# Performance work log

Measured on AMD Instinct MI355X. Metric: run time of the kernel, lower is better.

The kernel has to match this reference:

```python
import jax, jax.numpy as jnp
import numpy as np

B, N_IN, NV, F = 1, 65536, 1, 64
N_OUT, K = 16384, 16
N_DIST, N_PHI, OUT = 4, 8, 256
DIST_MAX = 0.1  # grid_layers[level_out].min_dist stand-in


def setup_inputs() -> dict:
    key = jax.random.key(0)
    ks = jax.random.split(key, 6)
    x = jax.random.normal(ks[0], (B, N_IN, NV, F), dtype=jnp.float32)
    nh_idx = jax.random.randint(ks[1], (N_OUT, K), 0, N_IN)  # neighbor gather indices
    d_dists = jax.random.uniform(ks[2], (N_OUT, K), dtype=jnp.float32) * DIST_MAX
    d_phi = jax.random.uniform(ks[3], (N_OUT, K), dtype=jnp.float32) * (2 * np.pi) - np.pi
    dists = jnp.linspace(0.0, DIST_MAX, N_DIST, dtype=jnp.float32)          # anchor distances
    sigma = jnp.asarray(DIST_MAX / 2, dtype=jnp.float32)                     # n_sigma == 1 -> scalar
    phi = jnp.linspace(-np.pi, np.pi, N_PHI + 1, dtype=jnp.float32)[:-1]     # von Mises: phi_min = -pi
    kappa = jnp.asarray(1.0, dtype=jnp.float32)                              # kappa_init
    W_out = jax.random.normal(ks[4], (F * N_DIST * N_PHI, OUT), dtype=jnp.float32) / np.sqrt(F * N_DIST * N_PHI)
    return {"x": x, "d_dists": d_dists, "d_phi": d_phi, "dists": dists,
            "sigma": sigma, "kappa": kappa, "phi": phi, "W_out": W_out, "nh_idx": nh_idx}


def reference(x, d_dists, d_phi, dists, sigma, kappa, phi, W_out, nh_idx):
    # Gaussian distance kernel: exp(-0.5*((d - dist_k)/sigma)^2)  -> (N_OUT, K, N_DIST)
    w_d = jnp.exp(-0.5 * ((d_dists[..., None] - dists) / sigma) ** 2)
    # von Mises angular kernel: exp(kappa * cos(d_phi - phi_p))   -> (N_OUT, K, N_PHI)
    w_p = jnp.exp(kappa * jnp.cos(d_phi[..., None] - phi))
    # combined kernel weights, normalized over the K neighbors per anchor
    w = w_d[..., :, None] * w_p[..., None, :]                      # (N_OUT, K, N_DIST, N_PHI)
    w = w / (jnp.sum(w, axis=1, keepdims=True) + 1e-9)
    w = w.reshape(N_OUT, K, N_DIST * N_PHI)                        # (N_OUT, K, M)
    # gather neighbor features from the input grid
    x_nb = x[:, nh_idx]                                            # (B, N_OUT, K, NV, F)
    # weighted aggregation over neighbors -> enhanced channels
    agg = jnp.einsum('bnkvf,nkm->bnvmf', x_nb, w)                  # (B, N_OUT, NV, M, F)
    agg = agg.reshape(B, N_OUT, NV, N_DIST * N_PHI * F)            # model_dim_enhanced = 2048
    return agg @ W_out                                             # (B, N_OUT, NV, OUT)
```

## Files before the change

### kernel.cpp

```cpp
#include <hip/hip_runtime.h>
#include <hip/hip_bf16.h>

#define N_IN   65536
#define N_OUTP 16384
#define KNB    16
#define FDIM   64
#define M_DIM  32
#define KDIM   2048
#define OUT_D  256

typedef __bf16 bf16x8_t __attribute__((ext_vector_type(8)));
typedef float  f32x4_t  __attribute__((ext_vector_type(4)));
typedef float  f32x2_t  __attribute__((ext_vector_type(2)));


__device__ __forceinline__ unsigned pk2(float a, float b) {
  __bf16 b0 = (__bf16)a, b1 = (__bf16)b;
  return ((unsigned)__builtin_bit_cast(unsigned short, b1) << 16) |
          (unsigned)__builtin_bit_cast(unsigned short, b0);
}

__global__ __launch_bounds__(256) void pack_B_kernel(
    const float* __restrict__ W, uint4* __restrict__ Bws)
{
  __shared__ float wlds[32 * 260];
  const int kk = blockIdx.x;
  const int t  = threadIdx.x;

  const float4* Wb = (const float4*)(W + kk * 32 * OUT_D);
#pragma unroll
  for (int i = 0; i < 8; ++i) {
    int idx = i * 256 + t;
    int row = idx >> 6, c4 = idx & 63;
    float4 v = Wb[idx];
    *(float4*)(wlds + row * 260 + c4 * 4) = v;
  }
  __syncthreads();

#pragma unroll
  for (int j = 0; j < 4; ++j) {
    int c  = j * 256 + t;
    int l  = c & 63, nt = c >> 6;
    int r0 = (l >> 4) * 8, col = nt * 16 + (l & 15);
    union { unsigned short s[8]; uint4 v; } u;
#pragma unroll
    for (int jj = 0; jj < 8; ++jj) {
      __bf16 b = (__bf16)wlds[(r0 + jj) * 260 + col];
      u.s[jj] = __builtin_bit_cast(unsigned short, b);
    }
    Bws[(size_t)kk * 1024 + c] = u.v;
  }
}

#define WST 580
#define WKS 36
#define XST 1092
#define XKS 68

__global__ __launch_bounds__(256) void agg_kernel(
    const float* __restrict__ x,
    const float* __restrict__ d_dists,
    const float* __restrict__ d_phi,
    const float* __restrict__ dists,
    const float* __restrict__ sigma_p,
    const float* __restrict__ kappa_p,
    const float* __restrict__ phi,
    const int*   __restrict__ nh_idx,
    uint4*       __restrict__ Aws)
{
  __shared__ __align__(16) float wbuf[8 * WST];
  __shared__ __align__(16) float xbuf[8 * XST];

  const int t  = threadIdx.x;
  const int n0 = blockIdx.x * 8;
  const int T  = blockIdx.x >> 1;
  const int r0 = (blockIdx.x & 1) * 8;

  const int h = t & 1, gk = (t >> 1) & 15, gr8 = t >> 5;
  const int gidx = nh_idx[(n0 + gr8) * KNB + gk];
  const float4* xr = (const float4*)x + (size_t)gidx * 16 + h * 8;
  float4 xreg[8];
#pragma unroll
  for (int j = 0; j < 8; ++j) xreg[j] = xr[j];

  {
    const float sinv = 1.0f / sigma_p[0];
    const float kap  = kappa_p[0];
    float phiv[8], distv[4];
#pragma unroll
    for (int p = 0; p < 8; ++p) phiv[p] = phi[p];
#pragma unroll
    for (int d = 0; d < 4; ++d) distv[d] = dists[d];

    int rk = t >> 1, r8 = rk >> 4, k = rk & 15, rep = t & 1;
    int n = n0 + r8;
    float dd = d_dists[n * KNB + k];
    float dp = d_phi[n * KNB + k];
    float wp[8];
#pragma unroll
    for (int p = 0; p < 8; ++p) wp[p] = __expf(kap * __cosf(dp - phiv[p]));
#pragma unroll
    for (int dl = 0; dl < 2; ++dl) {
      int d = rep * 2 + dl;
      float td = (dd - distv[d]) * sinv;
      float wd = __expf(-0.5f * td * td);
      float* dst = wbuf + r8 * WST + k * WKS + d * 8;
      *(float4*)(dst)     = make_float4(wd * wp[0], wd * wp[1], wd * wp[2], wd * wp[3]);
      *(float4*)(dst + 4) = make_float4(wd * wp[4], wd * wp[5], wd * wp[6], wd * wp[7]);
    }
  }

  {
    float4* xd = (float4*)(xbuf + gr8 * XST + gk * XKS + h * 36);
#pragma unroll
    for (int j = 0; j < 8; ++j) xd[j] = xreg[j];
  }
  __syncthreads();

  {
    int r8 = t >> 5, m = t & 31;
    float wv[16];
    float s = 0.f;
#pragma unroll
    for (int k = 0; k < 16; ++k) {
      wv[k] = wbuf[r8 * WST + k * WKS + m];
      s += wv[k];
    }
    float wn = 1.0f / (s + 1e-9f);
#pragma unroll
    for (int k = 0; k < 16; ++k)
      wbuf[r8 * WST + k * WKS + m] = wv[k] * wn;
  }
  __syncthreads();

  {
    const int r8 = t & 7, fo = (t >> 3) & 7, mq = t >> 6;
    f32x2_t acc[8][4];
#pragma unroll
    for (int mi = 0; mi < 8; ++mi)
#pragma unroll
      for (int fj = 0; fj < 4; ++fj) acc[mi][fj] = (f32x2_t){0.f, 0.f};

    const float* wp_ = wbuf + r8 * WST + mq * 8;
    const float* xp_ = xbuf + r8 * XST + ((fo < 4) ? fo * 8 : 36 + (fo - 4) * 8);

#pragma unroll 8
    for (int k = 0; k < 16; ++k) {
      float4 wa = *(const float4*)(wp_ + k * WKS);
      float4 wb = *(const float4*)(wp_ + k * WKS + 4);
      float4 xa = *(const float4*)(xp_ + k * XKS);
      float4 xb = *(const float4*)(xp_ + k * XKS + 4);
      float wv[8] = {wa.x, wa.y, wa.z, wa.w, wb.x, wb.y, wb.z, wb.w};
      f32x2_t xv[4] = {(f32x2_t){xa.x, xa.y}, (f32x2_t){xa.z, xa.w},
                       (f32x2_t){xb.x, xb.y}, (f32x2_t){xb.z, xb.w}};
#pragma unroll
      for (int mi = 0; mi < 8; ++mi) {
        f32x2_t wm = (f32x2_t){wv[mi], wv[mi]};
#pragma unroll
        for (int fj = 0; fj < 4; ++fj)
          acc[mi][fj] += wm * xv[fj];
      }
    }

    uint4* base = Aws + (size_t)T * 4096 + (fo & 3) * 16 + r0 + r8
                      + (size_t)(fo >> 2) * 64;
#pragma unroll
    for (int mi = 0; mi < 8; ++mi) {
      int m = mq * 8 + mi;
      uint4 v;
      v.x = pk2(acc[mi][0][0], acc[mi][0][1]);
      v.y = pk2(acc[mi][1][0], acc[mi][1][1]);
      v.z = pk2(acc[mi][2][0], acc[mi][2][1]);
      v.w = pk2(acc[mi][3][0], acc[mi][3][1]);
      base[m * 128] = v;
    }
  }
}

__global__ __launch_bounds__(512, 2) void gemm_kernel(
    const uint4* __restrict__ Astream,
    const uint4* __restrict__ Bws,
    float*       __restrict__ out)
{
  __shared__ float red[4][64 * 68];

  const int t    = threadIdx.x;
  const int lane = t & 63;
  const int w    = t >> 6;
  const int cg   = w & 3;
  const int half = w >> 2;
  const int rb   = blockIdx.x;

  const uint4* pa = Astream + (size_t)(rb * 4) * 4096 + half * 64 + lane;
  const uint4* pb = Bws + (half * 16 + cg * 4) * 64 + lane;

  f32x4_t cacc[4][4];
#pragma unroll
  for (int mt = 0; mt < 4; ++mt)
#pragma unroll
    for (int i = 0; i < 4; ++i)
      cacc[mt][i] = (f32x4_t){0.f, 0.f, 0.f, 0.f};

  uint4 a[4][4], b[4][4];
#pragma unroll
  for (int s = 0; s < 4; ++s) {
#pragma unroll
    for (int mt = 0; mt < 4; ++mt) a[s][mt] = pa[mt * 4096 + s * 128];
#pragma unroll
    for (int i = 0; i < 4; ++i)    b[s][i]  = pb[s * 2048 + i * 64];
  }

#pragma unroll 4
  for (int j = 0; j < 32; ++j) {
    const int s = j & 3;
    bf16x8_t B0 = __builtin_bit_cast(bf16x8_t, b[s][0]);
    bf16x8_t B1 = __builtin_bit_cast(bf16x8_t, b[s][1]);
    bf16x8_t B2 = __builtin_bit_cast(bf16x8_t, b[s][2]);
    bf16x8_t B3 = __builtin_bit_cast(bf16x8_t, b[s][3]);
#pragma unroll
    for (int mt = 0; mt < 4; ++mt) {
      bf16x8_t A = __builtin_bit_cast(bf16x8_t, a[s][mt]);
      cacc[mt][0] = __builtin_amdgcn_mfma_f32_16x16x32_bf16(A, B0, cacc[mt][0], 0, 0, 0);
      cacc[mt][1] = __builtin_amdgcn_mfma_f32_16x16x32_bf16(A, B1, cacc[mt][1], 0, 0, 0);
      cacc[mt][2] = __builtin_amdgcn_mfma_f32_16x16x32_bf16(A, B2, cacc[mt][2], 0, 0, 0);
      cacc[mt][3] = __builtin_amdgcn_mfma_f32_16x16x32_bf16(A, B3, cacc[mt][3], 0, 0, 0);
    }
    if (j < 28) {
#pragma unroll
      for (int mt = 0; mt < 4; ++mt) a[s][mt] = pa[mt * 4096 + (j + 4) * 128];
#pragma unroll
      for (int i = 0; i < 4; ++i)    b[s][i]  = pb[(j + 4) * 2048 + i * 64];
    }
  }

  const int lrow = (lane >> 4) * 4;
  const int lcol = lane & 15;

  if (half == 0) {
#pragma unroll
    for (int mt = 0; mt < 4; ++mt)
#pragma unroll
      for (int i = 0; i < 4; ++i)
#pragma unroll
        for (int reg = 0; reg < 4; ++reg)
          red[cg][(mt * 16 + lrow + reg) * 68 + i * 16 + lcol] = cacc[mt][i][reg];
  }
  __syncthreads();
  if (half == 1) {
#pragma unroll
    for (int mt = 0; mt < 4; ++mt)
#pragma unroll
      for (int i = 0; i < 4; ++i)
#pragma unroll
        for (int reg = 0; reg < 4; ++reg) {
          int row = mt * 16 + lrow + reg;
          int col = i * 16 + lcol;
          float v = red[cg][row * 68 + col] + cacc[mt][i][reg];
          out[(rb * 64 + row) * OUT_D + cg * 64 + col] = v;
        }
  }
}

extern "C" void kernel_launch(void* const* d_in, const int* in_sizes, int n_in,
                              void* d_out, int out_size, void* d_ws, size_t ws_size,
                              hipStream_t stream) {
  const float* x      = (const float*)d_in[0];
  const float* dd     = (const float*)d_in[1];
  const float* dp     = (const float*)d_in[2];
  const float* dists  = (const float*)d_in[3];
  const float* sigma  = (const float*)d_in[4];
  const float* kappa  = (const float*)d_in[5];
  const float* phi    = (const float*)d_in[6];
  const float* W      = (const float*)d_in[7];
  const int*   nh     = (const int*)d_in[8];
  float*       out    = (float*)d_out;

  uint4* Bws = (uint4*)d_ws;
  uint4* Aws = (uint4*)((char*)d_ws + (1 << 20));

  pack_B_kernel<<<64, 256, 0, stream>>>(W, Bws);
  agg_kernel<<<N_OUTP / 8, 256, 0, stream>>>(
      x, dd, dp, dists, sigma, kappa, phi, nh, Aws);
  gemm_kernel<<<N_OUTP / 64, 512, 0, stream>>>(Aws, Bws, out);
}
```

Baseline: 60.62 us.

## Stream gathered neighbor features from global memory directly into registers in agg kernel

```diff
diff --git a/kernel.cpp b/kernel.cpp
--- a/kernel.cpp
+++ b/kernel.cpp
@@ -54,8 +54,6 @@
 
 #define WST 580
 #define WKS 36
-#define XST 1092
-#define XKS 68
 
 __global__ __launch_bounds__(256) void agg_kernel(
     const float* __restrict__ x,
@@ -69,20 +67,13 @@
     uint4*       __restrict__ Aws)
 {
   __shared__ __align__(16) float wbuf[8 * WST];
-  __shared__ __align__(16) float xbuf[8 * XST];
+  __shared__ int idxb[8 * 16];
 
   const int t  = threadIdx.x;
   const int n0 = blockIdx.x * 8;
   const int T  = blockIdx.x >> 1;
   const int r0 = (blockIdx.x & 1) * 8;
 
-  const int h = t & 1, gk = (t >> 1) & 15, gr8 = t >> 5;
-  const int gidx = nh_idx[(n0 + gr8) * KNB + gk];
-  const float4* xr = (const float4*)x + (size_t)gidx * 16 + h * 8;
-  float4 xreg[8];
-#pragma unroll
-  for (int j = 0; j < 8; ++j) xreg[j] = xr[j];
-
   {
     const float sinv = 1.0f / sigma_p[0];
     const float kap  = kappa_p[0];
@@ -92,8 +83,8 @@
 #pragma unroll
     for (int d = 0; d < 4; ++d) distv[d] = dists[d];
 
-    int rk = t >> 1, r8 = rk >> 4, k = rk & 15, rep = t & 1;
-    int n = n0 + r8;
+    int rk = t >> 1, r8w = rk >> 4, k = rk & 15, rep = t & 1;
+    int n = n0 + r8w;
     float dd = d_dists[n * KNB + k];
     float dp = d_phi[n * KNB + k];
     float wp[8];
@@ -104,37 +95,48 @@
       int d = rep * 2 + dl;
       float td = (dd - distv[d]) * sinv;
       float wd = __expf(-0.5f * td * td);
-      float* dst = wbuf + r8 * WST + k * WKS + d * 8;
+      float* dst = wbuf + r8w * WST + k * WKS + d * 8;
       *(float4*)(dst)     = make_float4(wd * wp[0], wd * wp[1], wd * wp[2], wd * wp[3]);
       *(float4*)(dst + 4) = make_float4(wd * wp[4], wd * wp[5], wd * wp[6], wd * wp[7]);
     }
+    if (t < 128) {
+      int r8b = t >> 4, kb = t & 15;
+      idxb[r8b * 16 + kb] = nh_idx[(n0 + r8b) * KNB + kb];
+    }
+  }
+  __syncthreads();
+
+  const int r8 = t & 7, fo = (t >> 3) & 7, mq = t >> 6;
+
+  const float4* x4 = (const float4*)x;
+  int addr[16];
+#pragma unroll
+  for (int k = 0; k < 16; ++k)
+    addr[k] = idxb[r8 * 16 + k] * 16 + fo * 2;
+  float4 xa[4], xb[4];
+#pragma unroll
+  for (int s = 0; s < 4; ++s) {
+    xa[s] = x4[addr[s]];
+    xb[s] = x4[addr[s] + 1];
   }
 
   {
-    float4* xd = (float4*)(xbuf + gr8 * XST + gk * XKS + h * 36);
-#pragma unroll
-    for (int j = 0; j < 8; ++j) xd[j] = xreg[j];
-  }
-  __syncthreads();
-
-  {
-    int r8 = t >> 5, m = t & 31;
+    int nr8 = t >> 5, m = t & 31;
     float wv[16];
     float s = 0.f;
 #pragma unroll
     for (int k = 0; k < 16; ++k) {
-      wv[k] = wbuf[r8 * WST + k * WKS + m];
+      wv[k] = wbuf[nr8 * WST + k * WKS + m];
       s += wv[k];
     }
     float wn = 1.0f / (s + 1e-9f);
 #pragma unroll
     for (int k = 0; k < 16; ++k)
-      wbuf[r8 * WST + k * WKS + m] = wv[k] * wn;
+      wbuf[nr8 * WST + k * WKS + m] = wv[k] * wn;
   }
   __syncthreads();
 
   {
-    const int r8 = t & 7, fo = (t >> 3) & 7, mq = t >> 6;
     f32x2_t acc[8][4];
 #pragma unroll
     for (int mi = 0; mi < 8; ++mi)
@@ -142,17 +144,20 @@
       for (int fj = 0; fj < 4; ++fj) acc[mi][fj] = (f32x2_t){0.f, 0.f};
 
     const float* wp_ = wbuf + r8 * WST + mq * 8;
-    const float* xp_ = xbuf + r8 * XST + ((fo < 4) ? fo * 8 : 36 + (fo - 4) * 8);
-
-#pragma unroll 8
+
+#pragma unroll
     for (int k = 0; k < 16; ++k) {
+      const int s = k & 3;
+      float4 XA = xa[s], XB = xb[s];
+      if (k < 12) {
+        xa[s] = x4[addr[k + 4]];
+        xb[s] = x4[addr[k + 4] + 1];
+      }
       float4 wa = *(const float4*)(wp_ + k * WKS);
       float4 wb = *(const float4*)(wp_ + k * WKS + 4);
-      float4 xa = *(const float4*)(xp_ + k * XKS);
-      float4 xb = *(const float4*)(xp_ + k * XKS + 4);
       float wv[8] = {wa.x, wa.y, wa.z, wa.w, wb.x, wb.y, wb.z, wb.w};
-      f32x2_t xv[4] = {(f32x2_t){xa.x, xa.y}, (f32x2_t){xa.z, xa.w},
-                       (f32x2_t){xb.x, xb.y}, (f32x2_t){xb.z, xb.w}};
+      f32x2_t xv[4] = {(f32x2_t){XA.x, XA.y}, (f32x2_t){XA.z, XA.w},
+                       (f32x2_t){XB.x, XB.y}, (f32x2_t){XB.z, XB.w}};
 #pragma unroll
       for (int mi = 0; mi < 8; ++mi) {
         f32x2_t wm = (f32x2_t){wv[mi], wv[mi]};
```

New measurement: 67.79 us. 1.12x slower.

## Fuse neighbor aggregation and output GEMM into one kernel via LDS

Applied to the files above, without the earlier changes.

```diff
diff --git a/kernel.cpp b/kernel.cpp
--- a/kernel.cpp
+++ b/kernel.cpp
@@ -1,23 +1,24 @@
 #include <hip/hip_runtime.h>
 #include <hip/hip_bf16.h>
 
-#define N_IN   65536
 #define N_OUTP 16384
 #define KNB    16
-#define FDIM   64
-#define M_DIM  32
-#define KDIM   2048
 #define OUT_D  256
 
 typedef __bf16 bf16x8_t __attribute__((ext_vector_type(8)));
 typedef float  f32x4_t  __attribute__((ext_vector_type(4)));
 typedef float  f32x2_t  __attribute__((ext_vector_type(2)));
-
 
 __device__ __forceinline__ unsigned pk2(float a, float b) {
   __bf16 b0 = (__bf16)a, b1 = (__bf16)b;
   return ((unsigned)__builtin_bit_cast(unsigned short, b1) << 16) |
           (unsigned)__builtin_bit_cast(unsigned short, b0);
+}
+__device__ __forceinline__ float ulo(unsigned u) {
+  return __builtin_bit_cast(float, u << 16);
+}
+__device__ __forceinline__ float uhi(unsigned u) {
+  return __builtin_bit_cast(float, u & 0xffff0000u);
 }
 
 __global__ __launch_bounds__(256) void pack_B_kernel(
@@ -52,12 +53,14 @@
   }
 }
 
-#define WST 580
-#define WKS 36
-#define XST 1092
-#define XKS 68
-
-__global__ __launch_bounds__(256) void agg_kernel(
+#define XPK_OFF 0
+#define XPK_R   580
+#define WB_OFF  74240
+#define WB_R    324
+#define AC_OFF  115712
+#define LDS_TOT 148480
+
+__global__ __launch_bounds__(512) void fused_kernel(
     const float* __restrict__ x,
     const float* __restrict__ d_dists,
     const float* __restrict__ d_phi,
@@ -65,23 +68,24 @@
     const float* __restrict__ sigma_p,
     const float* __restrict__ kappa_p,
     const float* __restrict__ phi,
+    const uint4* __restrict__ Bws,
     const int*   __restrict__ nh_idx,
-    uint4*       __restrict__ Aws)
+    float*       __restrict__ out)
 {
-  __shared__ __align__(16) float wbuf[8 * WST];
-  __shared__ __align__(16) float xbuf[8 * XST];
+  extern __shared__ char smem[];
+  unsigned* xpk = (unsigned*)(smem + XPK_OFF);
+  unsigned* wb  = (unsigned*)(smem + WB_OFF);
+  uint4*    ac  = (uint4*)(smem + AC_OFF);
 
   const int t  = threadIdx.x;
-  const int n0 = blockIdx.x * 8;
-  const int T  = blockIdx.x >> 1;
-  const int r0 = (blockIdx.x & 1) * 8;
-
-  const int h = t & 1, gk = (t >> 1) & 15, gr8 = t >> 5;
-  const int gidx = nh_idx[(n0 + gr8) * KNB + gk];
-  const float4* xr = (const float4*)x + (size_t)gidx * 16 + h * 8;
-  float4 xreg[8];
-#pragma unroll
-  for (int j = 0; j < 8; ++j) xreg[j] = xr[j];
+  const int n0 = blockIdx.x * 32;
+
+  const int gr = t >> 4, gk = t & 15;
+  const int gidx = nh_idx[n0 * KNB + t];
+  const float4* xr = (const float4*)x + (size_t)gidx * 16;
+  float4 xreg[16];
+#pragma unroll
+  for (int j = 0; j < 16; ++j) xreg[j] = xr[j];
 
   {
     const float sinv = 1.0f / sigma_p[0];
@@ -92,171 +96,186 @@
 #pragma unroll
     for (int d = 0; d < 4; ++d) distv[d] = dists[d];
 
-    int rk = t >> 1, r8 = rk >> 4, k = rk & 15, rep = t & 1;
-    int n = n0 + r8;
-    float dd = d_dists[n * KNB + k];
-    float dp = d_phi[n * KNB + k];
+    float dd = d_dists[n0 * KNB + t];
+    float dp = d_phi[n0 * KNB + t];
     float wp[8];
 #pragma unroll
     for (int p = 0; p < 8; ++p) wp[p] = __expf(kap * __cosf(dp - phiv[p]));
-#pragma unroll
-    for (int dl = 0; dl < 2; ++dl) {
-      int d = rep * 2 + dl;
+
+    unsigned* wrow = wb + gr * WB_R + gk * 20;
+#pragma unroll
+    for (int d = 0; d < 4; ++d) {
       float td = (dd - distv[d]) * sinv;
       float wd = __expf(-0.5f * td * td);
-      float* dst = wbuf + r8 * WST + k * WKS + d * 8;
-      *(float4*)(dst)     = make_float4(wd * wp[0], wd * wp[1], wd * wp[2], wd * wp[3]);
-      *(float4*)(dst + 4) = make_float4(wd * wp[4], wd * wp[5], wd * wp[6], wd * wp[7]);
+      uint4 v;
+      v.x = pk2(wd * wp[0], wd * wp[1]);
+      v.y = pk2(wd * wp[2], wd * wp[3]);
+      v.z = pk2(wd * wp[4], wd * wp[5]);
+      v.w = pk2(wd * wp[6], wd * wp[7]);
+      *(uint4*)(wrow + d * 4) = v;
     }
   }
 
   {
-    float4* xd = (float4*)(xbuf + gr8 * XST + gk * XKS + h * 36);
-#pragma unroll
-    for (int j = 0; j < 8; ++j) xd[j] = xreg[j];
+    unsigned* xrow = xpk + gr * XPK_R + gk * 36;
+#pragma unroll
+    for (int q = 0; q < 8; ++q) {
+      float4 a = xreg[2 * q], b = xreg[2 * q + 1];
+      uint4 v;
+      v.x = pk2(a.x, a.y);
+      v.y = pk2(a.z, a.w);
+      v.z = pk2(b.x, b.y);
+      v.w = pk2(b.z, b.w);
+      *(uint4*)(xrow + q * 4) = v;
+    }
   }
   __syncthreads();
 
   {
-    int r8 = t >> 5, m = t & 31;
-    float wv[16];
-    float s = 0.f;
+    int r = t & 31, mp = t >> 5;
+    unsigned* col = wb + r * WB_R + mp;
+    unsigned v[16];
+    float s0 = 0.f, s1 = 0.f;
 #pragma unroll
     for (int k = 0; k < 16; ++k) {
-      wv[k] = wbuf[r8 * WST + k * WKS + m];
-      s += wv[k];
-    }
-    float wn = 1.0f / (s + 1e-9f);
+      v[k] = col[k * 20];
+      s0 += ulo(v[k]);
+      s1 += uhi(v[k]);
+    }
+    float i0 = 1.0f / (s0 + 1e-9f);
+    float i1 = 1.0f / (s1 + 1e-9f);
 #pragma unroll
     for (int k = 0; k < 16; ++k)
-      wbuf[r8 * WST + k * WKS + m] = wv[k] * wn;
+      col[k * 20] = pk2(ulo(v[k]) * i0, uhi(v[k]) * i1);
   }
   __syncthreads();
 
-  {
-    const int r8 = t & 7, fo = (t >> 3) & 7, mq = t >> 6;
-    f32x2_t acc[8][4];
-#pragma unroll
-    for (int mi = 0; mi < 8; ++mi)
+  const int lane = t & 63;
+  const int wv   = t >> 6;
+  const int cg   = wv & 3;
+  const int half = wv >> 2;
+
+  const int er  = t & 31;
+  const int efo = (t >> 5) & 7;
+  const int ems = t >> 8;
+
+  f32x4_t cacc[2][4];
+#pragma unroll
+  for (int mt = 0; mt < 2; ++mt)
+#pragma unroll
+    for (int i = 0; i < 4; ++i)
+      cacc[mt][i] = (f32x4_t){0.f, 0.f, 0.f, 0.f};
+
+  uint4 bpre[2][4];
+
+  for (int d = 0; d < 4; ++d) {
+#pragma unroll
+    for (int s = 0; s < 2; ++s) {
+      const uint4* pb = Bws + (size_t)(d * 16 + 2 * s + half) * 1024
+                            + (cg * 4) * 64 + lane;
+#pragma unroll
+      for (int i = 0; i < 4; ++i) bpre[s][i] = pb[i * 64];
+    }
+
+    f32x2_t acc[4][4];
+#pragma unroll
+    for (int mi = 0; mi < 4; ++mi)
 #pragma unroll
       for (int fj = 0; fj < 4; ++fj) acc[mi][fj] = (f32x2_t){0.f, 0.f};
 
-    const float* wp_ = wbuf + r8 * WST + mq * 8;
-    const float* xp_ = xbuf + r8 * XST + ((fo < 4) ? fo * 8 : 36 + (fo - 4) * 8);
+    const unsigned* xr_ = xpk + er * XPK_R + efo * 4;
+    const unsigned* wr_ = wb + er * WB_R + d * 4 + ems * 2;
 
 #pragma unroll 8
     for (int k = 0; k < 16; ++k) {
-      float4 wa = *(const float4*)(wp_ + k * WKS);
-      float4 wb = *(const float4*)(wp_ + k * WKS + 4);
-      float4 xa = *(const float4*)(xp_ + k * XKS);
-      float4 xb = *(const float4*)(xp_ + k * XKS + 4);
-      float wv[8] = {wa.x, wa.y, wa.z, wa.w, wb.x, wb.y, wb.z, wb.w};
-      f32x2_t xv[4] = {(f32x2_t){xa.x, xa.y}, (f32x2_t){xa.z, xa.w},
-                       (f32x2_t){xb.x, xb.y}, (f32x2_t){xb.z, xb.w}};
-#pragma unroll
-      for (int mi = 0; mi < 8; ++mi) {
-        f32x2_t wm = (f32x2_t){wv[mi], wv[mi]};
+      uint4 xu = *(const uint4*)(xr_ + k * 36);
+      unsigned w0 = wr_[k * 20], w1 = wr_[k * 20 + 1];
+      float wm[4] = {ulo(w0), uhi(w0), ulo(w1), uhi(w1)};
+      f32x2_t xv[4];
+      xv[0] = (f32x2_t){ulo(xu.x), uhi(xu.x)};
+      xv[1] = (f32x2_t){ulo(xu.y), uhi(xu.y)};
+      xv[2] = (f32x2_t){ulo(xu.z), uhi(xu.z)};
+      xv[3] = (f32x2_t){ulo(xu.w), uhi(xu.w)};
+#pragma unroll
+      for (int mi = 0; mi < 4; ++mi) {
+        f32x2_t wmm = (f32x2_t){wm[mi], wm[mi]};
 #pragma unroll
         for (int fj = 0; fj < 4; ++fj)
-          acc[mi][fj] += wm * xv[fj];
+          acc[mi][fj] += wmm * xv[fj];
       }
     }
 
-    uint4* base = Aws + (size_t)T * 4096 + (fo & 3) * 16 + r0 + r8
-                      + (size_t)(fo >> 2) * 64;
-#pragma unroll
-    for (int mi = 0; mi < 8; ++mi) {
-      int m = mq * 8 + mi;
-      uint4 v;
-      v.x = pk2(acc[mi][0][0], acc[mi][0][1]);
-      v.y = pk2(acc[mi][1][0], acc[mi][1][1]);
-      v.z = pk2(acc[mi][2][0], acc[mi][2][1]);
-      v.w = pk2(acc[mi][3][0], acc[mi][3][1]);
-      base[m * 128] = v;
-    }
-  }
-}
-
-__global__ __launch_bounds__(512, 2) void gemm_kernel(
-    const uint4* __restrict__ Astream,
-    const uint4* __restrict__ Bws,
-    float*       __restrict__ out)
-{
-  __shared__ float red[4][64 * 68];
-
-  const int t    = threadIdx.x;
-  const int lane = t & 63;
-  const int w    = t >> 6;
-  const int cg   = w & 3;
-  const int half = w >> 2;
-  const int rb   = blockIdx.x;
-
-  const uint4* pa = Astream + (size_t)(rb * 4) * 4096 + half * 64 + lane;
-  const uint4* pb = Bws + (half * 16 + cg * 4) * 64 + lane;
-
-  f32x4_t cacc[4][4];
-#pragma unroll
-  for (int mt = 0; mt < 4; ++mt)
-#pragma unroll
-    for (int i = 0; i < 4; ++i)
-      cacc[mt][i] = (f32x4_t){0.f, 0.f, 0.f, 0.f};
-
-  uint4 a[4][4], b[4][4];
-#pragma unroll
-  for (int s = 0; s < 4; ++s) {
-#pragma unroll
-    for (int mt = 0; mt < 4; ++mt) a[s][mt] = pa[mt * 4096 + s * 128];
-#pragma unroll
-    for (int i = 0; i < 4; ++i)    b[s][i]  = pb[s * 2048 + i * 64];
-  }
-
-#pragma unroll 4
-  for (int j = 0; j < 32; ++j) {
-    const int s = j & 3;
-    bf16x8_t B0 = __builtin_bit_cast(bf16x8_t, b[s][0]);
-    bf16x8_t B1 = __builtin_bit_cast(bf16x8_t, b[s][1]);
-    bf16x8_t B2 = __builtin_bit_cast(bf16x8_t, b[s][2]);
-    bf16x8_t B3 = __builtin_bit_cast(bf16x8_t, b[s][3]);
-#pragma unroll
-    for (int mt = 0; mt < 4; ++mt) {
-      bf16x8_t A = __builtin_bit_cast(bf16x8_t, a[s][mt]);
-      cacc[mt][0] = __builtin_amdgcn_mfma_f32_16x16x32_bf16(A, B0, cacc[mt][0], 0, 0, 0);
-      cacc[mt][1] = __builtin_amdgcn_mfma_f32_16x16x32_bf16(A, B1, cacc[mt][1], 0, 0, 0);
-      cacc[mt][2] = __builtin_amdgcn_mfma_f32_16x16x32_bf16(A, B2, cacc[mt][2], 0, 0, 0);
-      cacc[mt][3] = __builtin_amdgcn_mfma_f32_16x16x32_bf16(A, B3, cacc[mt][3], 0, 0, 0);
-    }
-    if (j < 28) {
-#pragma unroll
-      for (int mt = 0; mt < 4; ++mt) a[s][mt] = pa[mt * 4096 + (j + 4) * 128];
-#pragma unroll
-      for (int i = 0; i < 4; ++i)    b[s][i]  = pb[(j + 4) * 2048 + i * 64];
-    }
-  }
-
+    {
+      const int mt_   = er >> 4;
+      const int lane_ = (er & 15) + ((efo & 3) << 4);
+      const int kb    = efo >> 2;
+#pragma unroll
+      for (int mi = 0; mi < 4; ++mi) {
+        int m_l = ems * 4 + mi;
+        int kkl = m_l * 2 + kb;
+        uint4 v;
+        v.x = pk2(acc[mi][0][0], acc[mi][0][1]);
+        v.y = pk2(acc[mi][1][0], acc[mi][1][1]);
+        v.z = pk2(acc[mi][2][0], acc[mi][2][1]);
+        v.w = pk2(acc[mi][3][0], acc[mi][3][1]);
+        ac[(mt_ * 16 + kkl) * 64 + lane_] = v;
+      }
+    }
+    __syncthreads();
+
+#pragma unroll
+    for (int j = 0; j < 8; ++j) {
+      const int s   = j & 1;
+      const int kkl = 2 * j + half;
+      uint4 A0 = ac[kkl * 64 + lane];
+      uint4 A1 = ac[(16 + kkl) * 64 + lane];
+      uint4 bcur[4];
+#pragma unroll
+      for (int i = 0; i < 4; ++i) bcur[i] = bpre[s][i];
+      if (j < 6) {
+        const uint4* pb = Bws + (size_t)(d * 16 + 2 * (j + 2) + half) * 1024
+                              + (cg * 4) * 64 + lane;
+#pragma unroll
+        for (int i = 0; i < 4; ++i) bpre[s][i] = pb[i * 64];
+      }
+      bf16x8_t a0 = __builtin_bit_cast(bf16x8_t, A0);
+      bf16x8_t a1 = __builtin_bit_cast(bf16x8_t, A1);
+#pragma unroll
+      for (int i = 0; i < 4; ++i) {
+        bf16x8_t b = __builtin_bit_cast(bf16x8_t, bcur[i]);
+        cacc[0][i] = __builtin_amdgcn_mfma_f32_16x16x32_bf16(a0, b, cacc[0][i], 0, 0, 0);
+        cacc[1][i] = __builtin_amdgcn_mfma_f32_16x16x32_bf16(a1, b, cacc[1][i], 0, 0, 0);
+      }
+    }
+    __syncthreads();
+  }
+
+  float* red = (float*)(smem + XPK_OFF);
   const int lrow = (lane >> 4) * 4;
   const int lcol = lane & 15;
 
   if (half == 0) {
 #pragma unroll
-    for (int mt = 0; mt < 4; ++mt)
+    for (int mt = 0; mt < 2; ++mt)
 #pragma unroll
       for (int i = 0; i < 4; ++i)
 #pragma unroll
         for (int reg = 0; reg < 4; ++reg)
-          red[cg][(mt * 16 + lrow + reg) * 68 + i * 16 + lcol] = cacc[mt][i][reg];
+          red[(cg * 32 + mt * 16 + lrow + reg) * 68 + i * 16 + lcol] =
+              cacc[mt][i][reg];
   }
   __syncthreads();
   if (half == 1) {
 #pragma unroll
-    for (int mt = 0; mt < 4; ++mt)
+    for (int mt = 0; mt < 2; ++mt)
 #pragma unroll
       for (int i = 0; i < 4; ++i)
 #pragma unroll
         for (int reg = 0; reg < 4; ++reg) {
           int row = mt * 16 + lrow + reg;
           int col = i * 16 + lcol;
-          float v = red[cg][row * 68 + col] + cacc[mt][i][reg];
-          out[(rb * 64 + row) * OUT_D + cg * 64 + col] = v;
+          float v = red[(cg * 32 + row) * 68 + col] + cacc[mt][i][reg];
+          out[(n0 + row) * OUT_D + cg * 64 + col] = v;
         }
   }
 }
@@ -276,10 +295,11 @@
   float*       out    = (float*)d_out;
 
   uint4* Bws = (uint4*)d_ws;
-  uint4* Aws = (uint4*)((char*)d_ws + (1 << 20));
 
   pack_B_kernel<<<64, 256, 0, stream>>>(W, Bws);
-  agg_kernel<<<N_OUTP / 8, 256, 0, stream>>>(
-      x, dd, dp, dists, sigma, kappa, phi, nh, Aws);
-  gemm_kernel<<<N_OUTP / 64, 512, 0, stream>>>(Aws, Bws, out);
-}
+
+  hipFuncSetAttribute((const void*)fused_kernel,
+                      hipFuncAttributeMaxDynamicSharedMemorySize, LDS_TOT);
+  fused_kernel<<<N_OUTP / 32, 512, LDS_TOT, stream>>>(
+      x, dd, dp, dists, sigma, kappa, phi, Bws, nh, out);
+}
```

After: 80.01 us. 1.32x slower.
